# Optimization experiments

Measured on AMD Instinct MI355X. Metric: run time of the kernel, lower is better.

## Reference

```python
import jax, jax.numpy as jnp
import numpy as np

REPARAM_OFFSET = 2.0 ** -18
PEDESTAL = REPARAM_OFFSET ** 2            # 2**-36
BETA_MIN = 1e-6
BOUND_BETA = float(np.sqrt(BETA_MIN + PEDESTAL))
BOUND_A = float(np.sqrt(0.0 + PEDESTAL))


def nn_reparam(p, bound):
    # NonNegativeParametrizer.forward: lower_bound(p, bound)**2 - pedestal
    return jnp.maximum(p, bound) ** 2 - PEDESTAL


def setup_inputs() -> dict:
    key = jax.random.key(0)
    kx, ka = jax.random.split(key)
    C, R = 192, 8
    x = jax.random.normal(kx, (8, C, 256, 256), dtype=jnp.float32)
    # parameters stored in reparam-init space: init(v) = sqrt(max(v + ped, ped))
    beta = jnp.sqrt(jnp.ones((C,), jnp.float32) + PEDESTAL)
    A = jnp.sqrt(0.1 * jax.random.uniform(ka, (C, R), dtype=jnp.float32) + PEDESTAL)
    return {"x": x, "beta": beta, "A": A}


def reference(x, beta, A):
    beta_r = nn_reparam(beta, BOUND_BETA)[None, :, None, None]   # [1,C,1,1]
    A_r = nn_reparam(A, BOUND_A)                                  # [C,r]
    x2 = x * x
    T = jnp.einsum('nchw,cr->nrhw', x2, A_r)                      # low-rank projection
    denom_sq = jnp.einsum('cr,nrhw->nchw', A_r, T) + beta_r
    return x * jax.lax.rsqrt(denom_sq)                            # inverse=False -> rsqrt
```

## Files before the change

kernel.cpp:

```cpp
#include <hip/hip_runtime.h>


#define N_IMG 8
#define C_CH 192
#define R_RK 8
#define HW 65536
#define PX_PER_BLOCK 64
#define CSLICES 8
#define CPT (C_CH / CSLICES)
#define NTHR (PX_PER_BLOCK * CSLICES)
#define BLOCKS_PER_IMG (HW / PX_PER_BLOCK)

#define PEDESTAL_F 1.4551915228366852e-11f
#define BOUND_A_F 3.814697265625e-06f
#define BOUND_BETA_F 1.0000072759311364e-03f

__global__ __launch_bounds__(NTHR, 8) void lrgdn_kernel(
    const float* __restrict__ x,
    const float* __restrict__ beta,
    const float* __restrict__ A,
    float* __restrict__ out)
{
    __shared__ float sA[C_CH][R_RK];
    __shared__ float sB[C_CH];
    __shared__ float sT[CSLICES][R_RK][PX_PER_BLOCK];

    const int tid = threadIdx.x;

    for (int i = tid; i < C_CH * R_RK; i += NTHR) {
        float a = A[i];
        a = fmaxf(a, BOUND_A_F);
        sA[i / R_RK][i % R_RK] = a * a - PEDESTAL_F;
    }
    for (int i = tid; i < C_CH; i += NTHR) {
        float b = fmaxf(beta[i], BOUND_BETA_F);
        sB[i] = b * b - PEDESTAL_F;
    }
    __syncthreads();

    const int blk = blockIdx.x;
    const int n  = blk / BLOCKS_PER_IMG;
    const int p0 = (blk % BLOCKS_PER_IMG) * PX_PER_BLOCK;

    const int px = tid & 63;
    const int cs = tid >> 6;
    const int c0 = cs * CPT;

    const float* xn = x   + n * (C_CH * HW) + p0 + px + c0 * HW;
    float*       on = out + n * (C_CH * HW) + p0 + px + c0 * HW;

    float xr[CPT];
    float T[R_RK];
#pragma unroll
    for (int r = 0; r < R_RK; ++r) T[r] = 0.f;

#pragma unroll
    for (int i = 0; i < CPT; ++i) {
        xr[i] = xn[i * HW];
    }
#pragma unroll
    for (int i = 0; i < CPT; ++i) {
        float v = xr[i];
        float s = v * v;
#pragma unroll
        for (int r = 0; r < R_RK; ++r) {
            T[r] = fmaf(s, sA[c0 + i][r], T[r]);
        }
    }

#pragma unroll
    for (int r = 0; r < R_RK; ++r) {
        sT[cs][r][px] = T[r];
    }
    __syncthreads();

    float Tf[R_RK];
#pragma unroll
    for (int r = 0; r < R_RK; ++r) {
        float t01 = sT[0][r][px] + sT[1][r][px];
        float t23 = sT[2][r][px] + sT[3][r][px];
        float t45 = sT[4][r][px] + sT[5][r][px];
        float t67 = sT[6][r][px] + sT[7][r][px];
        Tf[r] = (t01 + t23) + (t45 + t67);
    }

#pragma unroll
    for (int i = 0; i < CPT; ++i) {
        int c = c0 + i;
        float d = sB[c];
#pragma unroll
        for (int r = 0; r < R_RK; ++r) {
            d = fmaf(sA[c][r], Tf[r], d);
        }
        float o = xr[i] * __builtin_amdgcn_rsqf(d);
        __builtin_nontemporal_store(o, on + i * HW);
    }
}

extern "C" void kernel_launch(void* const* d_in, const int* in_sizes, int n_in,
                              void* d_out, int out_size, void* d_ws, size_t ws_size,
                              hipStream_t stream) {
    const float* x    = (const float*)d_in[0];
    const float* beta = (const float*)d_in[1];
    const float* A    = (const float*)d_in[2];
    float* out = (float*)d_out;

    dim3 grid(N_IMG * BLOCKS_PER_IMG);
    dim3 block(NTHR);
    hipLaunchKernelGGL(lrgdn_kernel, grid, block, 0, stream, x, beta, A, out);
}
```

Before: 167.1 us.

## Process two pixels per thread with float2 loads and two-stage LDS reduction

Each thread now handles two adjacent pixels using float2 vector loads and stores, doubling pixels per block to 128 and halving the grid. The cross-slice reduction becomes a two-stage tree: the upper half of the slices fold into the lower half, then every thread sums four partials. Packed float2 math may map to packed FMA instructions. The aim is fewer memory instructions, better amortisation of the per-block parameter setup, and less LDS traffic, at the cost of more registers and an extra barrier.

```diff
diff --git a/kernel.cpp b/kernel.cpp
--- a/kernel.cpp
+++ b/kernel.cpp
@@ -5,17 +5,19 @@
 #define C_CH 192
 #define R_RK 8
 #define HW 65536
-#define PX_PER_BLOCK 64
+#define PXB 128
 #define CSLICES 8
 #define CPT (C_CH / CSLICES)
-#define NTHR (PX_PER_BLOCK * CSLICES)
-#define BLOCKS_PER_IMG (HW / PX_PER_BLOCK)
+#define NTHR 512
+#define BLOCKS_PER_IMG (HW / PXB)
 
 #define PEDESTAL_F 1.4551915228366852e-11f
 #define BOUND_A_F 3.814697265625e-06f
 #define BOUND_BETA_F 1.0000072759311364e-03f
 
-__global__ __launch_bounds__(NTHR, 8) void lrgdn_kernel(
+typedef float v2 __attribute__((ext_vector_type(2)));
+
+__global__ __launch_bounds__(NTHR, 6) void lrgdn_kernel(
     const float* __restrict__ x,
     const float* __restrict__ beta,
     const float* __restrict__ A,
@@ -23,14 +25,13 @@
 {
     __shared__ float sA[C_CH][R_RK];
     __shared__ float sB[C_CH];
-    __shared__ float sT[CSLICES][R_RK][PX_PER_BLOCK];
+    __shared__ v2 sT[CSLICES][R_RK][64];
 
     const int tid = threadIdx.x;
 
     for (int i = tid; i < C_CH * R_RK; i += NTHR) {
-        float a = A[i];
-        a = fmaxf(a, BOUND_A_F);
-        sA[i / R_RK][i % R_RK] = a * a - PEDESTAL_F;
+        float a = fmaxf(A[i], BOUND_A_F);
+        sA[i >> 3][i & 7] = a * a - PEDESTAL_F;
     }
     for (int i = tid; i < C_CH; i += NTHR) {
         float b = fmaxf(beta[i], BOUND_BETA_F);
@@ -38,62 +39,71 @@
     }
     __syncthreads();
 
-    const int blk = blockIdx.x;
-    const int n  = blk / BLOCKS_PER_IMG;
-    const int p0 = (blk % BLOCKS_PER_IMG) * PX_PER_BLOCK;
+    const int blk  = blockIdx.x;
+    const int n    = blk / BLOCKS_PER_IMG;
+    const int p0   = (blk % BLOCKS_PER_IMG) * PXB;
+    const int lane = tid & 63;
+    const int cs   = tid >> 6;
+    const int c0   = cs * CPT;
 
-    const int px = tid & 63;
-    const int cs = tid >> 6;
-    const int c0 = cs * CPT;
+    const float* xn = x   + (size_t)n * (C_CH * HW) + p0 + (size_t)c0 * HW + 2 * lane;
+    float*       on = out + (size_t)n * (C_CH * HW) + p0 + (size_t)c0 * HW + 2 * lane;
 
-    const float* xn = x   + n * (C_CH * HW) + p0 + px + c0 * HW;
-    float*       on = out + n * (C_CH * HW) + p0 + px + c0 * HW;
+    v2 xr[CPT];
+#pragma unroll
+    for (int i = 0; i < CPT; ++i) {
+        xr[i] = *reinterpret_cast<const v2*>(xn + (size_t)i * HW);
+    }
 
-    float xr[CPT];
-    float T[R_RK];
+    v2 T[R_RK];
 #pragma unroll
-    for (int r = 0; r < R_RK; ++r) T[r] = 0.f;
+    for (int r = 0; r < R_RK; ++r) T[r] = (v2)0.f;
 
 #pragma unroll
     for (int i = 0; i < CPT; ++i) {
-        xr[i] = xn[i * HW];
-    }
-#pragma unroll
-    for (int i = 0; i < CPT; ++i) {
-        float v = xr[i];
-        float s = v * v;
+        v2 s = xr[i] * xr[i];
 #pragma unroll
         for (int r = 0; r < R_RK; ++r) {
-            T[r] = fmaf(s, sA[c0 + i][r], T[r]);
+            T[r] += s * sA[c0 + i][r];
         }
     }
 
 #pragma unroll
     for (int r = 0; r < R_RK; ++r) {
-        sT[cs][r][px] = T[r];
+        sT[cs][r][lane] = T[r];
     }
     __syncthreads();
 
-    float Tf[R_RK];
+    if (cs < 4) {
+#pragma unroll
+        for (int r = 0; r < R_RK; ++r) {
+            T[r] += sT[cs + 4][r][lane];
+            sT[cs][r][lane] = T[r];
+        }
+    }
+    __syncthreads();
+
 #pragma unroll
     for (int r = 0; r < R_RK; ++r) {
-        float t01 = sT[0][r][px] + sT[1][r][px];
-        float t23 = sT[2][r][px] + sT[3][r][px];
-        float t45 = sT[4][r][px] + sT[5][r][px];
-        float t67 = sT[6][r][px] + sT[7][r][px];
-        Tf[r] = (t01 + t23) + (t45 + t67);
+        v2 a01 = sT[0][r][lane] + sT[1][r][lane];
+        v2 a23 = sT[2][r][lane] + sT[3][r][lane];
+        T[r] = a01 + a23;
     }
 
 #pragma unroll
     for (int i = 0; i < CPT; ++i) {
         int c = c0 + i;
-        float d = sB[c];
+        v2 d;
+        d.x = sB[c];
+        d.y = d.x;
 #pragma unroll
         for (int r = 0; r < R_RK; ++r) {
-            d = fmaf(sA[c][r], Tf[r], d);
+            d += sA[c][r] * T[r];
         }
-        float o = xr[i] * __builtin_amdgcn_rsqf(d);
-        __builtin_nontemporal_store(o, on + i * HW);
+        v2 o;
+        o.x = xr[i].x * __builtin_amdgcn_rsqf(d.x);
+        o.y = xr[i].y * __builtin_amdgcn_rsqf(d.y);
+        __builtin_nontemporal_store(o, reinterpret_cast<v2*>(on + (size_t)i * HW));
     }
 }
 
```

Result: slower. 188.2 us (+12.6%).
